# Optimization experiments

Measured on AMD Instinct MI355X. Metric: run time of the kernel, lower is better.

## Reference

```python
import jax, jax.numpy as jnp
import numpy as np

B, T, D_MODEL, N_HEAD = 1, 2048, 768, 12
D_HEAD = D_MODEL // N_HEAD
D_HID = 4 * D_MODEL
EPS = 1e-6
ROPE_BASE = 10000.0


def _rms(x):
    # F.rms_norm with no learned weight (pre-norm, modded-nanogpt style)
    return x * jax.lax.rsqrt(jnp.mean(x * x, axis=-1, keepdims=True) + EPS)


def _rope(x, cos, sin):
    # x: (B, T, H, Dh); cos/sin: (1, T, 1, Dh//2)
    d = x.shape[-1] // 2
    x1, x2 = x[..., :d], x[..., d:]
    return jnp.concatenate([x1 * cos + x2 * sin, -x1 * sin + x2 * cos], axis=-1)


def setup_inputs() -> dict:
    key = jax.random.key(0)
    ks = jax.random.split(key, 11)
    w = lambda k, shape: (jax.random.normal(k, shape, jnp.float32) * 0.02)
    return {
        "x": jax.random.normal(ks[0], (B, T, D_MODEL), jnp.float32),
        "Wq": w(ks[1], (D_MODEL, D_MODEL)),
        "Wk": w(ks[2], (D_MODEL, D_MODEL)),
        "Wq2": w(ks[3], (D_MODEL, D_MODEL)),
        "Wk2": w(ks[4], (D_MODEL, D_MODEL)),
        "Wv": w(ks[5], (D_MODEL, D_MODEL)),
        "Wo": w(ks[6], (D_MODEL, D_MODEL)),
        "Wp1": w(ks[7], (D_HID, D_MODEL)),
        "Wp2": w(ks[8], (D_HID, D_MODEL)),
        "Wd": w(ks[9], (D_MODEL, D_HID)),
        "bd": jax.random.normal(ks[10], (D_MODEL,), jnp.float32) * 0.02,
    }


def reference(x, Wq, Wk, Wq2, Wk2, Wv, Wo, Wp1, Wp2, Wd, bd):
    Bb, Tt, C = x.shape
    H, Dh = N_HEAD, C // N_HEAD

    # --- CausalBilinearSelfAttention (pre-norm residual) ---
    h = _rms(x)
    proj = lambda W: (h @ W.T).reshape(Bb, Tt, H, Dh)
    q, k, q2, k2, v = proj(Wq), proj(Wk), proj(Wq2), proj(Wk2), proj(Wv)

    inv_freq = 1.0 / (ROPE_BASE ** (jnp.arange(0, Dh, 2, dtype=jnp.float32) / Dh))
    freqs = jnp.arange(Tt, dtype=jnp.float32)[:, None] * inv_freq[None, :]  # (T, Dh/2)
    cos = jnp.cos(freqs)[None, :, None, :]
    sin = jnp.sin(freqs)[None, :, None, :]
    q, k = _rope(q, cos, sin), _rope(k, cos, sin)
    q2, k2 = _rope(q2, cos, sin), _rope(k2, cos, sin)

    scores = jnp.einsum('bqhd,bkhd->bhqk', q, k)    # (B,H,T,T)
    scores2 = jnp.einsum('bqhd,bkhd->bhqk', q2, k2)  # (B,H,T,T)
    pattern = (scores / Dh) * (scores2 / Dh)
    causal = jnp.tril(jnp.ones((Tt, Tt), dtype=bool))
    pattern = jnp.where(causal, pattern, 0.0)
    z = jnp.einsum('bhqk,bkhd->bqhd', pattern, v).reshape(Bb, Tt, C)
    x = x + z @ Wo.T

    # --- BilinearLayer MLP (pre-norm residual) ---
    h2 = _rms(x)
    hidden = (h2 @ Wp1.T) * (h2 @ Wp2.T)
    x = x + (hidden @ Wd.T + bd)
    return x
```

## Files before the change

kernel.cpp:

```cpp
#include <hip/hip_runtime.h>
#include <hip/hip_bf16.h>

typedef __bf16 bf16;
typedef bf16 bf16x8 __attribute__((ext_vector_type(8)));
typedef float f32x4 __attribute__((ext_vector_type(4)));

#define MFMA16(a, b, c) __builtin_amdgcn_mfma_f32_16x16x32_bf16((a), (b), (c), 0, 0, 0)

static constexpr int TT    = 2048;
static constexpr int CC    = 768;
static constexpr int NHEAD = 12;
static constexpr int DHEAD = 64;

__device__ inline bf16x8 cvt8(const float4& a, const float4& b) {
    bf16x8 o;
    o[0] = (bf16)a.x; o[1] = (bf16)a.y; o[2] = (bf16)a.z; o[3] = (bf16)a.w;
    o[4] = (bf16)b.x; o[5] = (bf16)b.y; o[6] = (bf16)b.z; o[7] = (bf16)b.w;
    return o;
}

struct BPtrs { const float* p[5]; };

__global__ __launch_bounds__(256) void zero_f32(float* __restrict__ p) {
    int i = (blockIdx.x * 256 + threadIdx.x) * 4;
    *(f32x4*)(p + i) = f32x4{0.f, 0.f, 0.f, 0.f};
}

__global__ __launch_bounds__(256) void init_bias(const float* __restrict__ xmid,
                                                 const float* __restrict__ bd,
                                                 float* __restrict__ out) {
    int i4 = (blockIdx.x * 256 + threadIdx.x) * 4;
    int col = i4 % CC;
    float4 a = *(const float4*)(xmid + i4);
    float4 b = *(const float4*)(bd + col);
    *(float4*)(out + i4) = float4{a.x + b.x, a.y + b.y, a.z + b.z, a.w + b.w};
}

__global__ __launch_bounds__(256) void rope_table(float* __restrict__ cosT, float* __restrict__ sinT) {
    int i = blockIdx.x * 256 + threadIdx.x;
    int t = i >> 5, j = i & 31;
    float inv = 1.0f / powf(10000.0f, (float)(2 * j) / 64.0f);
    float f = (float)t * inv;
    cosT[i] = cosf(f);
    sinT[i] = sinf(f);
}

__global__ __launch_bounds__(256) void rmsnorm(const float* __restrict__ x, bf16* __restrict__ out) {
    int row = blockIdx.x;
    const float* xr = x + (long)row * CC;
    int tid = threadIdx.x;
    float v0 = xr[tid], v1 = xr[tid + 256], v2 = xr[tid + 512];
    float ss = v0 * v0 + v1 * v1 + v2 * v2;
    #pragma unroll
    for (int off = 32; off > 0; off >>= 1) ss += __shfl_down(ss, off);
    __shared__ float red[4];
    if ((tid & 63) == 0) red[tid >> 6] = ss;
    __syncthreads();
    float tot = red[0] + red[1] + red[2] + red[3];
    float sc = rsqrtf(tot * (1.0f / 768.0f) + 1e-6f);
    bf16* o = out + (long)row * CC;
    o[tid]       = (bf16)(v0 * sc);
    o[tid + 256] = (bf16)(v1 * sc);
    o[tid + 512] = (bf16)(v2 * sc);
}

template <int EPI, bool AF32, int BM, int BN, int SK>
__global__ __launch_bounds__(256) void gemm_bt(
    const void* __restrict__ Av, BPtrs Bp, int partRows,
    bf16* __restrict__ outb, float* __restrict__ outf,
    const float* __restrict__ res, const float* __restrict__ bias,
    int M, int N, int K)
{
    constexpr int BK = 64, LDR = 72;
    constexpr int WC = BN / 64, WR = 4 / WC, FM = BM / (WR * 16);
    constexpr int RA = BM / 32, RB = BN / 32;
    __shared__ bf16 Al[BM * LDR];
    __shared__ bf16 Bl[BN * LDR];

    const int tid = threadIdx.x, lane = tid & 63, wave = tid >> 6;
    const int wr = wave / WC, wc = wave % WC;
    const int l15 = lane & 15, lhi = lane >> 4;
    const int bm = blockIdx.x * BM, bn = blockIdx.y * BN;
    const int seg = bn / partRows;
    const float* Bbase = Bp.p[seg] + (long)(bn - seg * partRows) * K;

    const int srow = tid >> 3;
    const int scol = (tid & 7) * 8;

    const int kchunk = K / SK;
    const int koff   = (SK > 1) ? blockIdx.z * kchunk : 0;

    const bf16*  Ag  = (const bf16*)Av  + (long)(bm + srow) * K + koff + scol;
    const float* Agf = (const float*)Av + (long)(bm + srow) * K + koff + scol;
    const float* Bg  = Bbase + (long)srow * K + koff + scol;

    f32x4 acc[FM][4] = {};
    const int nk = kchunk / BK;

    bf16x8 ga[RA];
    float4 fa[RA][2];
    float4 fb[RB][2];
    auto LOAD = [&](int t) {
        #pragma unroll
        for (int i = 0; i < RA; ++i) {
            if constexpr (AF32) {
                const float* p = Agf + (long)i * 32 * K + t * BK;
                fa[i][0] = *(const float4*)(p);
                fa[i][1] = *(const float4*)(p + 4);
            } else {
                ga[i] = *(const bf16x8*)(Ag + (long)i * 32 * K + t * BK);
            }
        }
        #pragma unroll
        for (int i = 0; i < RB; ++i) {
            const float* p = Bg + (long)i * 32 * K + t * BK;
            fb[i][0] = *(const float4*)(p);
            fb[i][1] = *(const float4*)(p + 4);
        }
    };
    LOAD(0);

    for (int t = 0; t < nk; ++t) {
        __syncthreads();
        #pragma unroll
        for (int i = 0; i < RA; ++i) {
            if constexpr (AF32)
                *(bf16x8*)(&Al[(srow + i * 32) * LDR + scol]) = cvt8(fa[i][0], fa[i][1]);
            else
                *(bf16x8*)(&Al[(srow + i * 32) * LDR + scol]) = ga[i];
        }
        #pragma unroll
        for (int i = 0; i < RB; ++i)
            *(bf16x8*)(&Bl[(srow + i * 32) * LDR + scol]) = cvt8(fb[i][0], fb[i][1]);
        __syncthreads();
        if (t + 1 < nk) LOAD(t + 1);

        bf16x8 afr[FM][2], bfr[4][2];
        #pragma unroll
        for (int m = 0; m < FM; ++m)
            #pragma unroll
            for (int kk = 0; kk < 2; ++kk)
                afr[m][kk] = *(const bf16x8*)(&Al[(wr * FM * 16 + m * 16 + l15) * LDR + kk * 32 + lhi * 8]);
        #pragma unroll
        for (int n = 0; n < 4; ++n)
            #pragma unroll
            for (int kk = 0; kk < 2; ++kk)
                bfr[n][kk] = *(const bf16x8*)(&Bl[(wc * 64 + n * 16 + l15) * LDR + kk * 32 + lhi * 8]);
        #pragma unroll
        for (int kk = 0; kk < 2; ++kk)
            #pragma unroll
            for (int m = 0; m < FM; ++m)
                #pragma unroll
                for (int n = 0; n < 4; ++n)
                    acc[m][n] = MFMA16(afr[m][kk], bfr[n][kk], acc[m][n]);
    }

    #pragma unroll
    for (int m = 0; m < FM; ++m) {
        #pragma unroll
        for (int n = 0; n < 4; ++n) {
            int row0 = bm + wr * FM * 16 + m * 16 + lhi * 4;
            int col  = bn + wc * 64 + n * 16 + l15;
            #pragma unroll
            for (int r = 0; r < 4; ++r) {
                long idx = (long)(row0 + r) * N + col;
                float v = acc[m][n][r];
                if (EPI == 0) {
                    outb[idx] = (bf16)v;
                } else if (EPI == 1) {
                    outf[idx] = res[idx] + v;
                } else if (EPI == 2) {
                    outf[idx] = res[idx] + bias[col] + v;
                } else {
                    atomicAdd(&outf[idx], v);
                }
            }
        }
    }
}

__global__ __launch_bounds__(256) void gemm_mlp_up(
    const bf16* __restrict__ A, const float* __restrict__ B1, const float* __restrict__ B2,
    bf16* __restrict__ out, int M, int N, int K)
{
    constexpr int BK = 64, LDR = 72;
    __shared__ bf16 Al[64 * LDR];
    __shared__ bf16 B1l[64 * LDR];
    __shared__ bf16 B2l[64 * LDR];

    const int tid = threadIdx.x, lane = tid & 63, wave = tid >> 6;
    const int l15 = lane & 15, lhi = lane >> 4;
    const int bm = blockIdx.x * 64, bn = blockIdx.y * 64;

    const int srow = tid >> 3;
    const int scol = (tid & 7) * 8;

    const bf16*  Ag  = A  + (long)(bm + srow) * K + scol;
    const float* B1g = B1 + (long)(bn + srow) * K + scol;
    const float* B2g = B2 + (long)(bn + srow) * K + scol;

    f32x4 acc1[4] = {};
    f32x4 acc2[4] = {};
    const int nk = K / BK;

    bf16x8 ga[2];
    float4 f1[2][2], f2[2][2];
    auto LOAD = [&](int t) {
        #pragma unroll
        for (int i = 0; i < 2; ++i) {
            ga[i] = *(const bf16x8*)(Ag + (long)i * 32 * K + t * BK);
            const float* p1 = B1g + (long)i * 32 * K + t * BK;
            const float* p2 = B2g + (long)i * 32 * K + t * BK;
            f1[i][0] = *(const float4*)(p1); f1[i][1] = *(const float4*)(p1 + 4);
            f2[i][0] = *(const float4*)(p2); f2[i][1] = *(const float4*)(p2 + 4);
        }
    };
    LOAD(0);

    for (int t = 0; t < nk; ++t) {
        __syncthreads();
        #pragma unroll
        for (int i = 0; i < 2; ++i) {
            *(bf16x8*)(&Al[(srow + i * 32) * LDR + scol])  = ga[i];
            *(bf16x8*)(&B1l[(srow + i * 32) * LDR + scol]) = cvt8(f1[i][0], f1[i][1]);
            *(bf16x8*)(&B2l[(srow + i * 32) * LDR + scol]) = cvt8(f2[i][0], f2[i][1]);
        }
        __syncthreads();
        if (t + 1 < nk) LOAD(t + 1);

        bf16x8 a[2], b1[4][2], b2[4][2];
        #pragma unroll
        for (int kk = 0; kk < 2; ++kk)
            a[kk] = *(const bf16x8*)(&Al[(wave * 16 + l15) * LDR + kk * 32 + lhi * 8]);
        #pragma unroll
        for (int n = 0; n < 4; ++n)
            #pragma unroll
            for (int kk = 0; kk < 2; ++kk) {
                b1[n][kk] = *(const bf16x8*)(&B1l[(n * 16 + l15) * LDR + kk * 32 + lhi * 8]);
                b2[n][kk] = *(const bf16x8*)(&B2l[(n * 16 + l15) * LDR + kk * 32 + lhi * 8]);
            }
        #pragma unroll
        for (int kk = 0; kk < 2; ++kk)
            #pragma unroll
            for (int n = 0; n < 4; ++n) {
                acc1[n] = MFMA16(a[kk], b1[n][kk], acc1[n]);
                acc2[n] = MFMA16(a[kk], b2[n][kk], acc2[n]);
            }
    }

    #pragma unroll
    for (int n = 0; n < 4; ++n) {
        int row0 = bm + wave * 16 + lhi * 4;
        int col  = bn + n * 16 + l15;
        #pragma unroll
        for (int r = 0; r < 4; ++r)
            out[(long)(row0 + r) * N + col] = (bf16)(acc1[n][r] * acc2[n][r]);
    }
}

__global__ __launch_bounds__(192) void rope_apply(bf16* __restrict__ qkv,
                                                  const float* __restrict__ cosT,
                                                  const float* __restrict__ sinT) {
    int t = blockIdx.x;
    int u = threadIdx.x;
    int mat = u / 48, r = u % 48;
    int hh = r >> 2, j8 = r & 3;
    long base = (long)t * 3840 + mat * CC + hh * DHEAD + j8 * 8;
    bf16x8 x1 = *(const bf16x8*)(qkv + base);
    bf16x8 x2 = *(const bf16x8*)(qkv + base + 32);
    float cv[8], sv[8];
    *(float4*)&cv[0] = *(const float4*)(cosT + t * 32 + j8 * 8);
    *(float4*)&cv[4] = *(const float4*)(cosT + t * 32 + j8 * 8 + 4);
    *(float4*)&sv[0] = *(const float4*)(sinT + t * 32 + j8 * 8);
    *(float4*)&sv[4] = *(const float4*)(sinT + t * 32 + j8 * 8 + 4);
    bf16x8 o1, o2;
    #pragma unroll
    for (int e = 0; e < 8; ++e) {
        float a = (float)x1[e], b = (float)x2[e];
        o1[e] = (bf16)(a * cv[e] + b * sv[e]);
        o2[e] = (bf16)(-a * sv[e] + b * cv[e]);
    }
    *(bf16x8*)(qkv + base)      = o1;
    *(bf16x8*)(qkv + base + 32) = o2;
}

__global__ __launch_bounds__(256) void attn(const bf16* __restrict__ qkv, float* __restrict__ z) {
    constexpr int LDK = 72, LDV = 66;
    __shared__ bf16 Kl[64 * LDK];
    __shared__ bf16 K2l[64 * LDK];
    __shared__ bf16 Vt[64 * LDV];
    __shared__ bf16 Pl[4][16 * LDK];

    const int qt = 31 - blockIdx.x, h = blockIdx.y, s = blockIdx.z;
    const int nkt  = qt + 1;
    const int base = nkt >> 3, rem = nkt & 7;
    const int len  = base + (s < rem ? 1 : 0);
    if (len == 0) return;
    const int k0 = s * base + min(s, rem);

    const int tid = threadIdx.x, lane = tid & 63, wave = tid >> 6;
    const int l15 = lane & 15, lhi = lane >> 4;
    const int q0w = qt * 64 + wave * 16;

    const bf16* qbase = qkv + (long)(q0w + l15) * 3840 + h * DHEAD + lhi * 8;
    const bf16x8 qa0  = *(const bf16x8*)(qbase);
    const bf16x8 qa1  = *(const bf16x8*)(qbase + 32);
    const bf16x8 q2a0 = *(const bf16x8*)(qbase + 1536);
    const bf16x8 q2a1 = *(const bf16x8*)(qbase + 1536 + 32);

    f32x4 zacc[4] = {};

    const int trow = tid >> 3;
    const int tcol = (tid & 7) * 8;

    bf16x8 kvr[2], k2r[2], vvr[2];
    auto LOAD = [&](int kt) {
        #pragma unroll
        for (int r2 = 0; r2 < 2; ++r2) {
            const bf16* src = qkv + (long)(kt * 64 + r2 * 32 + trow) * 3840 + h * DHEAD + tcol;
            kvr[r2] = *(const bf16x8*)(src + 768);
            k2r[r2] = *(const bf16x8*)(src + 2304);
            vvr[r2] = *(const bf16x8*)(src + 3072);
        }
    };
    LOAD(k0);

    for (int kt = k0; kt < k0 + len; ++kt) {
        __syncthreads();
        #pragma unroll
        for (int r2 = 0; r2 < 2; ++r2) {
            int krow = r2 * 32 + trow;
            *(bf16x8*)(&Kl[krow * LDK + tcol])  = kvr[r2];
            *(bf16x8*)(&K2l[krow * LDK + tcol]) = k2r[r2];
            #pragma unroll
            for (int e = 0; e < 8; ++e) Vt[(tcol + e) * LDV + krow] = vvr[r2][e];
        }
        __syncthreads();
        if (kt + 1 < k0 + len) LOAD(kt + 1);

        f32x4 s1[4] = {}, s2[4] = {};
        #pragma unroll
        for (int nf = 0; nf < 4; ++nf) {
            bf16x8 kb0 = *(const bf16x8*)(&Kl[(nf * 16 + l15) * LDK + lhi * 8]);
            s1[nf] = MFMA16(qa0, kb0, s1[nf]);
            bf16x8 kb1 = *(const bf16x8*)(&Kl[(nf * 16 + l15) * LDK + 32 + lhi * 8]);
            s1[nf] = MFMA16(qa1, kb1, s1[nf]);
            bf16x8 k2b0 = *(const bf16x8*)(&K2l[(nf * 16 + l15) * LDK + lhi * 8]);
            s2[nf] = MFMA16(q2a0, k2b0, s2[nf]);
            bf16x8 k2b1 = *(const bf16x8*)(&K2l[(nf * 16 + l15) * LDK + 32 + lhi * 8]);
            s2[nf] = MFMA16(q2a1, k2b1, s2[nf]);
        }

        #pragma unroll
        for (int nf = 0; nf < 4; ++nf) {
            #pragma unroll
            for (int r = 0; r < 4; ++r) {
                int qg = q0w + lhi * 4 + r;
                int kg = kt * 64 + nf * 16 + l15;
                float p = (kg <= qg) ? s1[nf][r] * s2[nf][r] * (1.0f / 4096.0f) : 0.0f;
                Pl[wave][(lhi * 4 + r) * LDK + nf * 16 + l15] = (bf16)p;
            }
        }

        #pragma unroll
        for (int kk = 0; kk < 2; ++kk) {
            bf16x8 pa = *(const bf16x8*)(&Pl[wave][l15 * LDK + kk * 32 + lhi * 8]);
            #pragma unroll
            for (int f = 0; f < 4; ++f) {
                bf16x8 vb = *(const bf16x8*)(&Vt[(f * 16 + l15) * LDV + kk * 32 + lhi * 8]);
                zacc[f] = MFMA16(pa, vb, zacc[f]);
            }
        }
    }

    #pragma unroll
    for (int f = 0; f < 4; ++f) {
        #pragma unroll
        for (int r = 0; r < 4; ++r) {
            atomicAdd(&z[(long)(q0w + lhi * 4 + r) * CC + h * DHEAD + f * 16 + l15], zacc[f][r]);
        }
    }
}

extern "C" void kernel_launch(void* const* d_in, const int* in_sizes, int n_in,
                              void* d_out, int out_size, void* d_ws, size_t ws_size,
                              hipStream_t stream) {
    const float* x   = (const float*)d_in[0];
    const float* Wq  = (const float*)d_in[1];
    const float* Wk  = (const float*)d_in[2];
    const float* Wq2 = (const float*)d_in[3];
    const float* Wk2 = (const float*)d_in[4];
    const float* Wv  = (const float*)d_in[5];
    const float* Wo  = (const float*)d_in[6];
    const float* Wp1 = (const float*)d_in[7];
    const float* Wp2 = (const float*)d_in[8];
    const float* Wd  = (const float*)d_in[9];
    const float* bd  = (const float*)d_in[10];

    char* ws = (char*)d_ws;
    size_t off = 0;
    auto alloc = [&](size_t bytes) {
        void* p = ws + off;
        off += (bytes + 255) & ~(size_t)255;
        return p;
    };
    float* xmid  = (float*)alloc(2048l * 768 * 4);
    bf16*  h2    = (bf16*)alloc(2048l * 768 * 2);
    bf16*  hid   = (bf16*)alloc(2048l * 3072 * 2);
    bf16*  h1    = (bf16*)alloc(2048l * 768 * 2);
    float* cosT  = (float*)alloc(2048l * 32 * 4);
    float* sinT  = (float*)alloc(2048l * 32 * 4);
    bf16*  qkv   = (bf16*)alloc(2048l * 3840 * 2);
    float* zbuf  = (float*)hid;

    BPtrs BQKV = {{Wq, Wk, Wq2, Wk2, Wv}};
    BPtrs BWO  = {{Wo, Wo, Wo, Wo, Wo}};
    BPtrs BWD  = {{Wd, Wd, Wd, Wd, Wd}};

    rope_table<<<dim3(256), 256, 0, stream>>>(cosT, sinT);
    rmsnorm<<<dim3(2048), 256, 0, stream>>>(x, h1);
    gemm_bt<0, false, 64, 128, 1><<<dim3(32, 30), 256, 0, stream>>>(
        h1, BQKV, 768, qkv, nullptr, nullptr, nullptr, 2048, 3840, 768);
    rope_apply<<<dim3(2048), 192, 0, stream>>>(qkv, cosT, sinT);
    zero_f32<<<dim3(1536), 256, 0, stream>>>(zbuf);
    attn<<<dim3(32, 12, 8), 256, 0, stream>>>(qkv, zbuf);
    hipMemcpyAsync(xmid, x, 2048l * 768 * 4, hipMemcpyDeviceToDevice, stream);
    gemm_bt<3, true, 64, 64, 2><<<dim3(32, 12, 2), 256, 0, stream>>>(
        zbuf, BWO, 768, nullptr, xmid, nullptr, nullptr, 2048, 768, 768);
    rmsnorm<<<dim3(2048), 256, 0, stream>>>(xmid, h2);
    gemm_mlp_up<<<dim3(32, 48), 256, 0, stream>>>(h2, Wp1, Wp2, hid, 2048, 3072, 768);
    init_bias<<<dim3(1536), 256, 0, stream>>>(xmid, bd, (float*)d_out);
    gemm_bt<3, false, 64, 64, 2><<<dim3(32, 12, 2), 256, 0, stream>>>(
        hid, BWD, 768, nullptr, (float*)d_out, nullptr, nullptr, 2048, 768, 3072);
}
```

Baseline: 282.0 us.

## Pre-convert weights to bf16, fuse RoPE into QKV GEMM, retile attention and MLP

Adds one kernel that converts all nine weight matrices to bf16 in a single launch, so the GEMMs load bf16 B tiles instead of converting fp32 per tile. RoPE is applied in a new epilogue of the QKV GEMM, which now uses 128x128 tiles, and the separate rope_apply pass is removed. Attention moves to 512-thread blocks covering 128 queries with a 4-way key split, and applies the causal mask only on diagonal tiles. The MLP up-projection uses 64x128 tiles. The weight conversion is an extra pass over about 42 MB of fp32 weights on every call.

```diff
diff --git a/kernel.cpp b/kernel.cpp
--- a/kernel.cpp
+++ b/kernel.cpp
@@ -19,7 +19,21 @@
     return o;
 }
 
-struct BPtrs { const float* p[5]; };
+struct ConvArgs {
+    const float* src[9];
+    bf16*        dst[9];
+    int          n[9];
+};
+
+__global__ __launch_bounds__(256) void convert_w(ConvArgs args) {
+    int seg = blockIdx.y;
+    int n   = args.n[seg];
+    int i8  = (blockIdx.x * 256 + threadIdx.x) * 8;
+    if (i8 >= n) return;
+    const float4 a = *(const float4*)(args.src[seg] + i8);
+    const float4 b = *(const float4*)(args.src[seg] + i8 + 4);
+    *(bf16x8*)(args.dst[seg] + i8) = cvt8(a, b);
+}
 
 __global__ __launch_bounds__(256) void zero_f32(float* __restrict__ p) {
     int i = (blockIdx.x * 256 + threadIdx.x) * 4;
@@ -66,9 +80,10 @@
 
 template <int EPI, bool AF32, int BM, int BN, int SK>
 __global__ __launch_bounds__(256) void gemm_bt(
-    const void* __restrict__ Av, BPtrs Bp, int partRows,
+    const void* __restrict__ Av, const bf16* __restrict__ B,
     bf16* __restrict__ outb, float* __restrict__ outf,
     const float* __restrict__ res, const float* __restrict__ bias,
+    const float* __restrict__ cosT, const float* __restrict__ sinT,
     int M, int N, int K)
 {
     constexpr int BK = 64, LDR = 72;
@@ -81,8 +96,6 @@
     const int wr = wave / WC, wc = wave % WC;
     const int l15 = lane & 15, lhi = lane >> 4;
     const int bm = blockIdx.x * BM, bn = blockIdx.y * BN;
-    const int seg = bn / partRows;
-    const float* Bbase = Bp.p[seg] + (long)(bn - seg * partRows) * K;
 
     const int srow = tid >> 3;
     const int scol = (tid & 7) * 8;
@@ -92,14 +105,13 @@
 
     const bf16*  Ag  = (const bf16*)Av  + (long)(bm + srow) * K + koff + scol;
     const float* Agf = (const float*)Av + (long)(bm + srow) * K + koff + scol;
-    const float* Bg  = Bbase + (long)srow * K + koff + scol;
+    const bf16*  Bg  = B + (long)(bn + srow) * K + koff + scol;
 
     f32x4 acc[FM][4] = {};
     const int nk = kchunk / BK;
 
-    bf16x8 ga[RA];
+    bf16x8 ga[RA], gb[RB];
     float4 fa[RA][2];
-    float4 fb[RB][2];
     auto LOAD = [&](int t) {
         #pragma unroll
         for (int i = 0; i < RA; ++i) {
@@ -112,11 +124,8 @@
             }
         }
         #pragma unroll
-        for (int i = 0; i < RB; ++i) {
-            const float* p = Bg + (long)i * 32 * K + t * BK;
-            fb[i][0] = *(const float4*)(p);
-            fb[i][1] = *(const float4*)(p + 4);
-        }
+        for (int i = 0; i < RB; ++i)
+            gb[i] = *(const bf16x8*)(Bg + (long)i * 32 * K + t * BK);
     };
     LOAD(0);
 
@@ -131,7 +140,7 @@
         }
         #pragma unroll
         for (int i = 0; i < RB; ++i)
-            *(bf16x8*)(&Bl[(srow + i * 32) * LDR + scol]) = cvt8(fb[i][0], fb[i][1]);
+            *(bf16x8*)(&Bl[(srow + i * 32) * LDR + scol]) = gb[i];
         __syncthreads();
         if (t + 1 < nk) LOAD(t + 1);
 
@@ -153,6 +162,38 @@
                 #pragma unroll
                 for (int n = 0; n < 4; ++n)
                     acc[m][n] = MFMA16(afr[m][kk], bfr[n][kk], acc[m][n]);
+    }
+
+    if (EPI == 4) {
+        const bool dorope = (bn < 3072);
+        #pragma unroll
+        for (int m = 0; m < FM; ++m) {
+            int row0 = bm + wr * FM * 16 + m * 16 + lhi * 4;
+            if (dorope) {
+                #pragma unroll
+                for (int n = 0; n < 2; ++n) {
+                    int j   = n * 16 + l15;
+                    int col = bn + wc * 64 + n * 16 + l15;
+                    #pragma unroll
+                    for (int r = 0; r < 4; ++r) {
+                        int t = row0 + r;
+                        float c = cosT[t * 32 + j], s = sinT[t * 32 + j];
+                        float a = acc[m][n][r], b = acc[m][n + 2][r];
+                        outb[(long)t * N + col]      = (bf16)(a * c + b * s);
+                        outb[(long)t * N + col + 32] = (bf16)(-a * s + b * c);
+                    }
+                }
+            } else {
+                #pragma unroll
+                for (int n = 0; n < 4; ++n) {
+                    int col = bn + wc * 64 + n * 16 + l15;
+                    #pragma unroll
+                    for (int r = 0; r < 4; ++r)
+                        outb[(long)(row0 + r) * N + col] = (bf16)acc[m][n][r];
+                }
+            }
+        }
+        return;
     }
 
     #pragma unroll
@@ -180,39 +221,39 @@
 }
 
 __global__ __launch_bounds__(256) void gemm_mlp_up(
-    const bf16* __restrict__ A, const float* __restrict__ B1, const float* __restrict__ B2,
+    const bf16* __restrict__ A, const bf16* __restrict__ B1, const bf16* __restrict__ B2,
     bf16* __restrict__ out, int M, int N, int K)
 {
     constexpr int BK = 64, LDR = 72;
     __shared__ bf16 Al[64 * LDR];
-    __shared__ bf16 B1l[64 * LDR];
-    __shared__ bf16 B2l[64 * LDR];
+    __shared__ bf16 B1l[128 * LDR];
+    __shared__ bf16 B2l[128 * LDR];
 
     const int tid = threadIdx.x, lane = tid & 63, wave = tid >> 6;
+    const int wr = wave >> 1, wc = wave & 1;
     const int l15 = lane & 15, lhi = lane >> 4;
-    const int bm = blockIdx.x * 64, bn = blockIdx.y * 64;
+    const int bm = blockIdx.x * 64, bn = blockIdx.y * 128;
 
     const int srow = tid >> 3;
     const int scol = (tid & 7) * 8;
 
-    const bf16*  Ag  = A  + (long)(bm + srow) * K + scol;
-    const float* B1g = B1 + (long)(bn + srow) * K + scol;
-    const float* B2g = B2 + (long)(bn + srow) * K + scol;
-
-    f32x4 acc1[4] = {};
-    f32x4 acc2[4] = {};
+    const bf16* Ag  = A  + (long)(bm + srow) * K + scol;
+    const bf16* B1g = B1 + (long)(bn + srow) * K + scol;
+    const bf16* B2g = B2 + (long)(bn + srow) * K + scol;
+
+    f32x4 acc1[2][4] = {};
+    f32x4 acc2[2][4] = {};
     const int nk = K / BK;
 
-    bf16x8 ga[2];
-    float4 f1[2][2], f2[2][2];
+    bf16x8 ga[2], g1[4], g2[4];
     auto LOAD = [&](int t) {
         #pragma unroll
-        for (int i = 0; i < 2; ++i) {
+        for (int i = 0; i < 2; ++i)
             ga[i] = *(const bf16x8*)(Ag + (long)i * 32 * K + t * BK);
-            const float* p1 = B1g + (long)i * 32 * K + t * BK;
-            const float* p2 = B2g + (long)i * 32 * K + t * BK;
-            f1[i][0] = *(const float4*)(p1); f1[i][1] = *(const float4*)(p1 + 4);
-            f2[i][0] = *(const float4*)(p2); f2[i][1] = *(const float4*)(p2 + 4);
+        #pragma unroll
+        for (int i = 0; i < 4; ++i) {
+            g1[i] = *(const bf16x8*)(B1g + (long)i * 32 * K + t * BK);
+            g2[i] = *(const bf16x8*)(B2g + (long)i * 32 * K + t * BK);
         }
     };
     LOAD(0);
@@ -220,87 +261,71 @@
     for (int t = 0; t < nk; ++t) {
         __syncthreads();
         #pragma unroll
-        for (int i = 0; i < 2; ++i) {
-            *(bf16x8*)(&Al[(srow + i * 32) * LDR + scol])  = ga[i];
-            *(bf16x8*)(&B1l[(srow + i * 32) * LDR + scol]) = cvt8(f1[i][0], f1[i][1]);
-            *(bf16x8*)(&B2l[(srow + i * 32) * LDR + scol]) = cvt8(f2[i][0], f2[i][1]);
+        for (int i = 0; i < 2; ++i)
+            *(bf16x8*)(&Al[(srow + i * 32) * LDR + scol]) = ga[i];
+        #pragma unroll
+        for (int i = 0; i < 4; ++i) {
+            *(bf16x8*)(&B1l[(srow + i * 32) * LDR + scol]) = g1[i];
+            *(bf16x8*)(&B2l[(srow + i * 32) * LDR + scol]) = g2[i];
         }
         __syncthreads();
         if (t + 1 < nk) LOAD(t + 1);
 
-        bf16x8 a[2], b1[4][2], b2[4][2];
+        bf16x8 a[2][2], b1[4][2], b2[4][2];
+        #pragma unroll
+        for (int m = 0; m < 2; ++m)
+            #pragma unroll
+            for (int kk = 0; kk < 2; ++kk)
+                a[m][kk] = *(const bf16x8*)(&Al[(wr * 32 + m * 16 + l15) * LDR + kk * 32 + lhi * 8]);
+        #pragma unroll
+        for (int n = 0; n < 4; ++n)
+            #pragma unroll
+            for (int kk = 0; kk < 2; ++kk) {
+                b1[n][kk] = *(const bf16x8*)(&B1l[(wc * 64 + n * 16 + l15) * LDR + kk * 32 + lhi * 8]);
+                b2[n][kk] = *(const bf16x8*)(&B2l[(wc * 64 + n * 16 + l15) * LDR + kk * 32 + lhi * 8]);
+            }
         #pragma unroll
         for (int kk = 0; kk < 2; ++kk)
-            a[kk] = *(const bf16x8*)(&Al[(wave * 16 + l15) * LDR + kk * 32 + lhi * 8]);
-        #pragma unroll
-        for (int n = 0; n < 4; ++n)
-            #pragma unroll
-            for (int kk = 0; kk < 2; ++kk) {
-                b1[n][kk] = *(const bf16x8*)(&B1l[(n * 16 + l15) * LDR + kk * 32 + lhi * 8]);
-                b2[n][kk] = *(const bf16x8*)(&B2l[(n * 16 + l15) * LDR + kk * 32 + lhi * 8]);
-            }
-        #pragma unroll
-        for (int kk = 0; kk < 2; ++kk)
-            #pragma unroll
-            for (int n = 0; n < 4; ++n) {
-                acc1[n] = MFMA16(a[kk], b1[n][kk], acc1[n]);
-                acc2[n] = MFMA16(a[kk], b2[n][kk], acc2[n]);
-            }
+            #pragma unroll
+            for (int m = 0; m < 2; ++m)
+                #pragma unroll
+                for (int n = 0; n < 4; ++n) {
+                    acc1[m][n] = MFMA16(a[m][kk], b1[n][kk], acc1[m][n]);
+                    acc2[m][n] = MFMA16(a[m][kk], b2[n][kk], acc2[m][n]);
+                }
     }
 
     #pragma unroll
-    for (int n = 0; n < 4; ++n) {
-        int row0 = bm + wave * 16 + lhi * 4;
-        int col  = bn + n * 16 + l15;
-        #pragma unroll
-        for (int r = 0; r < 4; ++r)
-            out[(long)(row0 + r) * N + col] = (bf16)(acc1[n][r] * acc2[n][r]);
-    }
-}
-
-__global__ __launch_bounds__(192) void rope_apply(bf16* __restrict__ qkv,
-                                                  const float* __restrict__ cosT,
-                                                  const float* __restrict__ sinT) {
-    int t = blockIdx.x;
-    int u = threadIdx.x;
-    int mat = u / 48, r = u % 48;
-    int hh = r >> 2, j8 = r & 3;
-    long base = (long)t * 3840 + mat * CC + hh * DHEAD + j8 * 8;
-    bf16x8 x1 = *(const bf16x8*)(qkv + base);
-    bf16x8 x2 = *(const bf16x8*)(qkv + base + 32);
-    float cv[8], sv[8];
-    *(float4*)&cv[0] = *(const float4*)(cosT + t * 32 + j8 * 8);
-    *(float4*)&cv[4] = *(const float4*)(cosT + t * 32 + j8 * 8 + 4);
-    *(float4*)&sv[0] = *(const float4*)(sinT + t * 32 + j8 * 8);
-    *(float4*)&sv[4] = *(const float4*)(sinT + t * 32 + j8 * 8 + 4);
-    bf16x8 o1, o2;
-    #pragma unroll
-    for (int e = 0; e < 8; ++e) {
-        float a = (float)x1[e], b = (float)x2[e];
-        o1[e] = (bf16)(a * cv[e] + b * sv[e]);
-        o2[e] = (bf16)(-a * sv[e] + b * cv[e]);
-    }
-    *(bf16x8*)(qkv + base)      = o1;
-    *(bf16x8*)(qkv + base + 32) = o2;
-}
-
-__global__ __launch_bounds__(256) void attn(const bf16* __restrict__ qkv, float* __restrict__ z) {
-    constexpr int LDK = 72, LDV = 66;
+    for (int m = 0; m < 2; ++m) {
+        #pragma unroll
+        for (int n = 0; n < 4; ++n) {
+            int row0 = bm + wr * 32 + m * 16 + lhi * 4;
+            int col  = bn + wc * 64 + n * 16 + l15;
+            #pragma unroll
+            for (int r = 0; r < 4; ++r)
+                out[(long)(row0 + r) * N + col] = (bf16)(acc1[m][n][r] * acc2[m][n][r]);
+        }
+    }
+}
+
+__global__ __launch_bounds__(512) void attn(const bf16* __restrict__ qkv, float* __restrict__ z) {
+    constexpr int LDK = 72, LDV = 66, LDP = 72;
     __shared__ bf16 Kl[64 * LDK];
     __shared__ bf16 K2l[64 * LDK];
     __shared__ bf16 Vt[64 * LDV];
-    __shared__ bf16 Pl[4][16 * LDK];
-
-    const int qt = 31 - blockIdx.x, h = blockIdx.y, s = blockIdx.z;
-    const int nkt  = qt + 1;
-    const int base = nkt >> 3, rem = nkt & 7;
-    const int len  = base + (s < rem ? 1 : 0);
+    __shared__ bf16 Pl[8][16 * LDP];
+
+    const int qtb = 15 - blockIdx.x, h = blockIdx.y, s = blockIdx.z;
+    const int nkt = 2 * qtb + 2;
+    const int cb = nkt >> 2, rem = nkt & 3;
+    const int len = cb + (s < rem ? 1 : 0);
     if (len == 0) return;
-    const int k0 = s * base + min(s, rem);
+    const int k0 = s * cb + min(s, rem);
 
     const int tid = threadIdx.x, lane = tid & 63, wave = tid >> 6;
     const int l15 = lane & 15, lhi = lane >> 4;
-    const int q0w = qt * 64 + wave * 16;
+    const int q0w = qtb * 128 + wave * 16;
+    const int wkt0 = q0w >> 6;
 
     const bf16* qbase = qkv + (long)(q0w + l15) * 3840 + h * DHEAD + lhi * 8;
     const bf16x8 qa0  = *(const bf16x8*)(qbase);
@@ -310,33 +335,29 @@
 
     f32x4 zacc[4] = {};
 
-    const int trow = tid >> 3;
-    const int tcol = (tid & 7) * 8;
-
-    bf16x8 kvr[2], k2r[2], vvr[2];
+    const int srow = tid >> 3;
+    const int scol = (tid & 7) * 8;
+
+    bf16x8 kvr, k2r, vvr;
     auto LOAD = [&](int kt) {
-        #pragma unroll
-        for (int r2 = 0; r2 < 2; ++r2) {
-            const bf16* src = qkv + (long)(kt * 64 + r2 * 32 + trow) * 3840 + h * DHEAD + tcol;
-            kvr[r2] = *(const bf16x8*)(src + 768);
-            k2r[r2] = *(const bf16x8*)(src + 2304);
-            vvr[r2] = *(const bf16x8*)(src + 3072);
-        }
+        const bf16* src = qkv + (long)(kt * 64 + srow) * 3840 + h * DHEAD + scol;
+        kvr = *(const bf16x8*)(src + 768);
+        k2r = *(const bf16x8*)(src + 2304);
+        vvr = *(const bf16x8*)(src + 3072);
     };
     LOAD(k0);
 
     for (int kt = k0; kt < k0 + len; ++kt) {
         __syncthreads();
-        #pragma unroll
-        for (int r2 = 0; r2 < 2; ++r2) {
-            int krow = r2 * 32 + trow;
-            *(bf16x8*)(&Kl[krow * LDK + tcol])  = kvr[r2];
-            *(bf16x8*)(&K2l[krow * LDK + tcol]) = k2r[r2];
-            #pragma unroll
-            for (int e = 0; e < 8; ++e) Vt[(tcol + e) * LDV + krow] = vvr[r2][e];
-        }
+        *(bf16x8*)(&Kl[srow * LDK + scol])  = kvr;
+        *(bf16x8*)(&K2l[srow * LDK + scol]) = k2r;
+        #pragma unroll
+        for (int e = 0; e < 8; ++e) Vt[(scol + e) * LDV + srow] = vvr[e];
         __syncthreads();
         if (kt + 1 < k0 + len) LOAD(kt + 1);
+
+        if (kt > wkt0) continue;
+        const bool diag = (kt == wkt0);
 
         f32x4 s1[4] = {}, s2[4] = {};
         #pragma unroll
@@ -355,16 +376,19 @@
         for (int nf = 0; nf < 4; ++nf) {
             #pragma unroll
             for (int r = 0; r < 4; ++r) {
-                int qg = q0w + lhi * 4 + r;
-                int kg = kt * 64 + nf * 16 + l15;
-                float p = (kg <= qg) ? s1[nf][r] * s2[nf][r] * (1.0f / 4096.0f) : 0.0f;
-                Pl[wave][(lhi * 4 + r) * LDK + nf * 16 + l15] = (bf16)p;
+                float p = s1[nf][r] * s2[nf][r] * (1.0f / 4096.0f);
+                if (diag) {
+                    int qg = q0w + lhi * 4 + r;
+                    int kg = kt * 64 + nf * 16 + l15;
+                    p = (kg <= qg) ? p : 0.0f;
+                }
+                Pl[wave][(lhi * 4 + r) * LDP + nf * 16 + l15] = (bf16)p;
             }
         }
 
         #pragma unroll
         for (int kk = 0; kk < 2; ++kk) {
-            bf16x8 pa = *(const bf16x8*)(&Pl[wave][l15 * LDK + kk * 32 + lhi * 8]);
+            bf16x8 pa = *(const bf16x8*)(&Pl[wave][l15 * LDP + kk * 32 + lhi * 8]);
             #pragma unroll
             for (int f = 0; f < 4; ++f) {
                 bf16x8 vb = *(const bf16x8*)(&Vt[(f * 16 + l15) * LDV + kk * 32 + lhi * 8]);
@@ -373,11 +397,13 @@
         }
     }
 
-    #pragma unroll
-    for (int f = 0; f < 4; ++f) {
-        #pragma unroll
-        for (int r = 0; r < 4; ++r) {
-            atomicAdd(&z[(long)(q0w + lhi * 4 + r) * CC + h * DHEAD + f * 16 + l15], zacc[f][r]);
+    if (k0 <= wkt0) {
+        #pragma unroll
+        for (int f = 0; f < 4; ++f) {
+            #pragma unroll
+            for (int r = 0; r < 4; ++r) {
+                atomicAdd(&z[(long)(q0w + lhi * 4 + r) * CC + h * DHEAD + f * 16 + l15], zacc[f][r]);
+            }
         }
     }
 }
@@ -404,6 +430,7 @@
         off += (bytes + 255) & ~(size_t)255;
         return p;
     };
+    bf16*  Wall  = (bf16*)alloc(10616832l * 2);
     float* xmid  = (float*)alloc(2048l * 768 * 4);
     bf16*  h2    = (bf16*)alloc(2048l * 768 * 2);
     bf16*  hid   = (bf16*)alloc(2048l * 3072 * 2);
@@ -413,23 +440,33 @@
     bf16*  qkv   = (bf16*)alloc(2048l * 3840 * 2);
     float* zbuf  = (float*)hid;
 
-    BPtrs BQKV = {{Wq, Wk, Wq2, Wk2, Wv}};
-    BPtrs BWO  = {{Wo, Wo, Wo, Wo, Wo}};
-    BPtrs BWD  = {{Wd, Wd, Wd, Wd, Wd}};
-
+    const long SW = 589824;
+    bf16* Wqkvb = Wall;
+    bf16* Wob   = Wall + 5 * SW;
+    bf16* Wp1b  = Wall + 6 * SW;
+    bf16* Wp2b  = Wp1b + 2359296;
+    bf16* Wdb   = Wp2b + 2359296;
+
+    ConvArgs ca;
+    const float* wsrc[9] = {Wq, Wk, Wq2, Wk2, Wv, Wo, Wp1, Wp2, Wd};
+    bf16* wdst[9] = {Wqkvb, Wqkvb + SW, Wqkvb + 2 * SW, Wqkvb + 3 * SW, Wqkvb + 4 * SW,
+                     Wob, Wp1b, Wp2b, Wdb};
+    int wn[9] = {589824, 589824, 589824, 589824, 589824, 589824, 2359296, 2359296, 2359296};
+    for (int i = 0; i < 9; ++i) { ca.src[i] = wsrc[i]; ca.dst[i] = wdst[i]; ca.n[i] = wn[i]; }
+
+    convert_w<<<dim3(1152, 9), 256, 0, stream>>>(ca);
     rope_table<<<dim3(256), 256, 0, stream>>>(cosT, sinT);
     rmsnorm<<<dim3(2048), 256, 0, stream>>>(x, h1);
-    gemm_bt<0, false, 64, 128, 1><<<dim3(32, 30), 256, 0, stream>>>(
-        h1, BQKV, 768, qkv, nullptr, nullptr, nullptr, 2048, 3840, 768);
-    rope_apply<<<dim3(2048), 192, 0, stream>>>(qkv, cosT, sinT);
+    gemm_bt<4, false, 128, 128, 1><<<dim3(16, 30), 256, 0, stream>>>(
+        h1, Wqkvb, qkv, nullptr, nullptr, nullptr, cosT, sinT, 2048, 3840, 768);
     zero_f32<<<dim3(1536), 256, 0, stream>>>(zbuf);
-    attn<<<dim3(32, 12, 8), 256, 0, stream>>>(qkv, zbuf);
+    attn<<<dim3(16, 12, 4), 512, 0, stream>>>(qkv, zbuf);
     hipMemcpyAsync(xmid, x, 2048l * 768 * 4, hipMemcpyDeviceToDevice, stream);
     gemm_bt<3, true, 64, 64, 2><<<dim3(32, 12, 2), 256, 0, stream>>>(
-        zbuf, BWO, 768, nullptr, xmid, nullptr, nullptr, 2048, 768, 768);
+        zbuf, Wob, nullptr, xmid, nullptr, nullptr, nullptr, nullptr, 2048, 768, 768);
     rmsnorm<<<dim3(2048), 256, 0, stream>>>(xmid, h2);
-    gemm_mlp_up<<<dim3(32, 48), 256, 0, stream>>>(h2, Wp1, Wp2, hid, 2048, 3072, 768);
+    gemm_mlp_up<<<dim3(32, 24), 256, 0, stream>>>(h2, Wp1b, Wp2b, hid, 2048, 3072, 768);
     init_bias<<<dim3(1536), 256, 0, stream>>>(xmid, bd, (float*)d_out);
     gemm_bt<3, false, 64, 64, 2><<<dim3(32, 12, 2), 256, 0, stream>>>(
-        hid, BWD, 768, nullptr, (float*)d_out, nullptr, nullptr, 2048, 768, 3072);
-}
+        hid, Wdb, nullptr, (float*)d_out, nullptr, nullptr, nullptr, nullptr, 2048, 768, 3072);
+}
```

New measurement: 250.2 us. 1.13x faster.
